# Optimization experiments

Measured on AMD Instinct MI355X. Metric: run time of the kernel, lower is better.

## Reference

```python
import jax, jax.numpy as jnp
import numpy as np

LN_EPS = 1e-5

def layer_norm(x, g, b):
    mu = jnp.mean(x, axis=-1, keepdims=True)
    var = jnp.var(x, axis=-1, keepdims=True)
    return (x - mu) * jax.lax.rsqrt(var + LN_EPS) * g + b

def setup_inputs() -> dict:
    key = jax.random.key(0)
    ks = jax.random.split(key, 4)
    d = 2048
    bs, win_len, obj_num = 8, 64, 36
    return {
        "visual_feats": jax.random.normal(ks[0], (bs, win_len, d), dtype=jnp.float32),
        "obj_feats": jax.random.normal(ks[1], (bs, win_len, obj_num, d), dtype=jnp.float32),
        "W_v": jax.random.normal(ks[2], (d, d), dtype=jnp.float32) * (1.0 / np.sqrt(d)),
        "b_v": jnp.zeros((d,), dtype=jnp.float32),
        "W_o": jax.random.normal(ks[3], (d, d), dtype=jnp.float32) * (1.0 / np.sqrt(d)),
        "b_o": jnp.zeros((d,), dtype=jnp.float32),
        "ln_v_g": jnp.ones((d,), dtype=jnp.float32),
        "ln_v_b": jnp.zeros((d,), dtype=jnp.float32),
        "ln_o_g": jnp.ones((d,), dtype=jnp.float32),
        "ln_o_b": jnp.zeros((d,), dtype=jnp.float32),
        "ln_ov_g": jnp.ones((d,), dtype=jnp.float32),
        "ln_ov_b": jnp.zeros((d,), dtype=jnp.float32),
    }

def reference(visual_feats, obj_feats, W_v, b_v, W_o, b_o,
              ln_v_g, ln_v_b, ln_o_g, ln_o_b, ln_ov_g, ln_ov_b):
    bs, win_len, obj_num, obj_size = obj_feats.shape
    # visual branch: linear -> tanh -> LN   [bs, F, d]
    ve = layer_norm(jnp.tanh(visual_feats @ W_v + b_v), ln_v_g, ln_v_b)
    # object branch: linear -> flatten frames*objects -> tanh -> LN  [bs, N, d]
    oe = (obj_feats @ W_o + b_o).reshape(bs, win_len * obj_num, obj_size)
    oe = layer_norm(jnp.tanh(oe), ln_o_g, ln_o_b)
    # adjacency: [bs, N, F], softmax over N (object axis, dim=1)
    adj = jnp.einsum('bnd,bfd->bnf', oe, ve) / jnp.sqrt(jnp.asarray(obj_size, dtype=oe.dtype))
    adj = jax.nn.softmax(adj, axis=1)
    # aggregate objects per frame: (oe^T @ adj)^T -> [bs, F, d]
    obj_agg = jnp.einsum('bnd,bnf->bfd', oe, adj)
    return layer_norm(jnp.tanh(obj_agg + ve), ln_ov_g, ln_ov_b)
```

## Files before the change

### kernel.cpp

```cpp
#include <hip/hip_runtime.h>
#include <cstdint>
#include <cstddef>


typedef __attribute__((ext_vector_type(4))) float f32x4;
typedef __attribute__((ext_vector_type(4))) unsigned int u32x4;
typedef __attribute__((ext_vector_type(8))) short bf16x8;

#define DD 2048
#define BS 8
#define FF 64
#define NOBJ 2304
#define MO 18432
#define MV 512

__device__ __forceinline__ unsigned short f2bf(float f) {
  unsigned int u = __float_as_uint(f);
  u += 0x7fffu + ((u >> 16) & 1u);
  return (unsigned short)(u >> 16);
}
__device__ __forceinline__ unsigned int pk2(float a, float b) {
  return (unsigned int)f2bf(a) | ((unsigned int)f2bf(b) << 16);
}
__device__ __forceinline__ float bf2f(unsigned short u) {
  return __uint_as_float((unsigned int)u << 16);
}

typedef __attribute__((address_space(1))) const unsigned int gas_u32;
typedef __attribute__((address_space(3))) unsigned int las_u32;
__device__ __forceinline__ void gl_lds16(const void* g, void* l) {
  __builtin_amdgcn_global_load_lds((gas_u32*)g, (las_u32*)l, 16, 0, 0);
}

__global__ __launch_bounds__(256) void k_cvt_bf16(const float* __restrict__ X,
                                                  unsigned short* __restrict__ O,
                                                  int n16) {
  int idx = blockIdx.x * 256 + threadIdx.x;
  const int stride = gridDim.x * 256;
  for (int i = idx; i < n16; i += stride) {
    const f32x4* src = (const f32x4*)(X + (size_t)i * 16);
    f32x4 a = src[0], b = src[1], c = src[2], d = src[3];
    u32x4 p = {pk2(a.x, a.y), pk2(a.z, a.w), pk2(b.x, b.y), pk2(b.z, b.w)};
    u32x4 q = {pk2(c.x, c.y), pk2(c.z, c.w), pk2(d.x, d.y), pk2(d.z, d.w)};
    u32x4* dst = (u32x4*)(O + (size_t)i * 16);
    dst[0] = p;
    dst[1] = q;
  }
}

__global__ __launch_bounds__(256) void k_wprep(const float* __restrict__ W,
                                               unsigned short* __restrict__ Wt) {
  __shared__ unsigned short sh[64][65];
  const int t = threadIdx.x;
  const int kb = blockIdx.x * 64, nb = blockIdx.y * 64;
  {
    const int rk = t >> 2, seg = t & 3;
    const float* src = W + (size_t)(kb + rk) * DD + nb + seg * 16;
#pragma unroll
    for (int q = 0; q < 4; ++q) {
      f32x4 x = *(const f32x4*)(src + q * 4);
      sh[rk][seg * 16 + q * 4 + 0] = f2bf(x.x);
      sh[rk][seg * 16 + q * 4 + 1] = f2bf(x.y);
      sh[rk][seg * 16 + q * 4 + 2] = f2bf(x.z);
      sh[rk][seg * 16 + q * 4 + 3] = f2bf(x.w);
    }
  }
  __syncthreads();
  {
    const int nn = t >> 2, ks = t & 3;
    unsigned int o[8];
#pragma unroll
    for (int j = 0; j < 8; ++j)
      o[j] = (unsigned int)sh[ks * 16 + 2 * j][nn] |
             ((unsigned int)sh[ks * 16 + 2 * j + 1][nn] << 16);
    u32x4 p0 = {o[0], o[1], o[2], o[3]};
    u32x4 p1 = {o[4], o[5], o[6], o[7]};
    unsigned short* dst = Wt + (size_t)(nb + nn) * DD + kb + ks * 16;
    ((u32x4*)dst)[0] = p0;
    ((u32x4*)dst)[1] = p1;
  }
}

__global__ __launch_bounds__(512, 1) void k_gemm_bbf(const unsigned short* __restrict__ A,
                                                     const unsigned short* __restrict__ Bt,
                                                     const float* __restrict__ bias,
                                                     unsigned short* __restrict__ T,
                                                     float* __restrict__ part) {
  __shared__ __align__(16) unsigned short lds[2 * 32768];
  const int tid = threadIdx.x;
  const int lane = tid & 63, wave = tid >> 6;
  const int r = lane & 15, g = lane >> 4;
  const int wm = wave >> 2, wn = wave & 3;

  const int orig = blockIdx.y * 8 + blockIdx.x;
  const int lin = (orig & 7) * 72 + (orig >> 3);
  const int bm = (lin >> 3) * 256;
  const int bn = (lin & 7) * 256;

  const int srow = tid >> 3;
  const int k16s = (tid & 7) ^ (srow & 7);
  const unsigned short* aS = A + (size_t)(bm + srow) * DD + k16s * 8;
  const unsigned short* bS = Bt + (size_t)(bn + srow) * DD + k16s * 8;

  auto stage = [&](int buf, int kt) {
    unsigned short* ab = lds + buf * 32768;
    unsigned short* bb = ab + 16384;
    const size_t ko = (size_t)kt * 64;
#pragma unroll
    for (int i = 0; i < 4; ++i)
      gl_lds16(aS + ko + (size_t)(i * 64) * DD, ab + ((i * 512 + tid) << 3));
#pragma unroll
    for (int i = 0; i < 4; ++i)
      gl_lds16(bS + ko + (size_t)(i * 64) * DD, bb + ((i * 512 + tid) << 3));
  };

  const int rs = r & 7;
  const int s0 = ((0 + g) ^ rs) * 8;
  const int s1 = ((4 + g) ^ rs) * 8;
  const int abase = (wm * 128 + r) * 64;
  const int bbase = 16384 + (wn * 64 + r) * 64;

  f32x4 acc[8][4] = {};

  stage(0, 0);
  asm volatile("s_waitcnt vmcnt(0)" ::: "memory");
  __builtin_amdgcn_s_barrier();

  for (int kt = 0; kt < DD / 64; ++kt) {
    const unsigned short* bufp = lds + (kt & 1) * 32768;
    const bool st = (kt + 1 < DD / 64);

#define PHASE(QA, QB, DOSTAGE, DOWAIT)                                         \
    {                                                                          \
      bf16x8 af[4][2], bfv[2][2];                                              \
      _Pragma("unroll")                                                        \
      for (int mi = 0; mi < 4; ++mi) {                                         \
        const int ro = abase + ((QA) * 64 + mi * 16) * 64;                     \
        af[mi][0] = *(const bf16x8*)(bufp + ro + s0);                          \
        af[mi][1] = *(const bf16x8*)(bufp + ro + s1);                          \
      }                                                                        \
      _Pragma("unroll")                                                        \
      for (int ni = 0; ni < 2; ++ni) {                                         \
        const int ro = bbase + ((QB) * 32 + ni * 16) * 64;                     \
        bfv[ni][0] = *(const bf16x8*)(bufp + ro + s0);                         \
        bfv[ni][1] = *(const bf16x8*)(bufp + ro + s1);                         \
      }                                                                        \
      if (DOSTAGE) stage((kt + 1) & 1, kt + 1);                                \
      __builtin_amdgcn_s_barrier();                                            \
      __builtin_amdgcn_s_setprio(1);                                           \
      _Pragma("unroll")                                                        \
      for (int mi = 0; mi < 4; ++mi)                                           \
        _Pragma("unroll")                                                      \
        for (int ni = 0; ni < 2; ++ni) {                                       \
          acc[(QA) * 4 + mi][(QB) * 2 + ni] = __builtin_amdgcn_mfma_f32_16x16x32_bf16( \
              af[mi][0], bfv[ni][0], acc[(QA) * 4 + mi][(QB) * 2 + ni], 0, 0, 0);      \
          acc[(QA) * 4 + mi][(QB) * 2 + ni] = __builtin_amdgcn_mfma_f32_16x16x32_bf16( \
              af[mi][1], bfv[ni][1], acc[(QA) * 4 + mi][(QB) * 2 + ni], 0, 0, 0);      \
        }                                                                      \
      __builtin_amdgcn_s_setprio(0);                                           \
      if (DOWAIT) asm volatile("s_waitcnt vmcnt(0)" ::: "memory");             \
      __builtin_amdgcn_s_barrier();                                            \
    }

    PHASE(0, 0, st, false)
    PHASE(0, 1, false, false)
    PHASE(1, 0, false, false)
    PHASE(1, 1, false, st)
#undef PHASE
  }

  float bv[4];
#pragma unroll
  for (int ni = 0; ni < 4; ++ni) bv[ni] = bias[bn + wn * 64 + ni * 16 + r];
  const int slot = ((lin & 7) << 2) + wn;
#pragma unroll
  for (int mi = 0; mi < 8; ++mi) {
#pragma unroll
    for (int i2 = 0; i2 < 4; ++i2) {
      const int row = bm + wm * 128 + mi * 16 + g * 4 + i2;
      unsigned short* trow = T + (size_t)row * DD + bn + wn * 64 + r;
      float s1 = 0.f, s2 = 0.f;
#pragma unroll
      for (int ni = 0; ni < 4; ++ni) {
        const float tv = tanhf(acc[mi][ni][i2] + bv[ni]);
        trow[ni * 16] = f2bf(tv);
        s1 += tv;
        s2 += tv * tv;
      }
#pragma unroll
      for (int m = 1; m < 16; m <<= 1) {
        s1 += __shfl_xor(s1, m, 64);
        s2 += __shfl_xor(s2, m, 64);
      }
      if (r == 0) {
        float2 p2 = make_float2(s1, s2);
        *(float2*)(part + (size_t)row * 64 + slot * 2) = p2;
      }
    }
  }
}

__global__ __launch_bounds__(256) void k_ep_ln2(const unsigned short* __restrict__ T,
                                                const float* __restrict__ part,
                                                const float* __restrict__ gw,
                                                const float* __restrict__ bw,
                                                unsigned short* __restrict__ obf) {
  const int row = blockIdx.x, t = threadIdx.x;
  float s1 = 0.f, s2 = 0.f;
  if (t < 32) {
    float2 p = ((const float2*)(part + (size_t)row * 64))[t];
    s1 = p.x;
    s2 = p.y;
  }
#pragma unroll
  for (int m = 1; m < 64; m <<= 1) {
    s1 += __shfl_xor(s1, m, 64);
    s2 += __shfl_xor(s2, m, 64);
  }
  __shared__ float sh[2];
  if (t == 0) {
    sh[0] = s1;
    sh[1] = s2;
  }
  __syncthreads();
  const float mean = sh[0] * (1.0f / DD);
  const float var = sh[1] * (1.0f / DD) - mean * mean;
  const float rstd = rsqrtf(var + 1e-5f);
  const size_t base = (size_t)row * DD + t * 8;
  u32x4 tin = *(const u32x4*)(T + base);
  f32x4 g0 = ((const f32x4*)(gw + t * 8))[0], g1 = ((const f32x4*)(gw + t * 8))[1];
  f32x4 bb0 = ((const f32x4*)(bw + t * 8))[0], bb1 = ((const f32x4*)(bw + t * 8))[1];
  float gv[8], bvv[8];
  gv[0] = g0.x; gv[1] = g0.y; gv[2] = g0.z; gv[3] = g0.w;
  gv[4] = g1.x; gv[5] = g1.y; gv[6] = g1.z; gv[7] = g1.w;
  bvv[0] = bb0.x; bvv[1] = bb0.y; bvv[2] = bb0.z; bvv[3] = bb0.w;
  bvv[4] = bb1.x; bvv[5] = bb1.y; bvv[6] = bb1.z; bvv[7] = bb1.w;
  float o[8];
#pragma unroll
  for (int j = 0; j < 4; ++j) {
    const float tl = bf2f((unsigned short)(tin[j] & 0xffffu));
    const float th = bf2f((unsigned short)(tin[j] >> 16));
    o[2 * j] = (tl - mean) * rstd * gv[2 * j] + bvv[2 * j];
    o[2 * j + 1] = (th - mean) * rstd * gv[2 * j + 1] + bvv[2 * j + 1];
  }
  u32x4 p = {pk2(o[0], o[1]), pk2(o[2], o[3]), pk2(o[4], o[5]), pk2(o[6], o[7])};
  *((u32x4*)(obf + base)) = p;
}

__global__ __launch_bounds__(256) void k_gemm_xw(const float* __restrict__ X,
                                                 const unsigned short* __restrict__ Wt,
                                                 const float* __restrict__ bias,
                                                 float* __restrict__ Y) {
  __shared__ __align__(16) unsigned short As[128 * 32];
  __shared__ __align__(16) unsigned short Bs[128 * 32];
  const int t = threadIdx.x;
  const int lane = t & 63, wave = t >> 6;
  const int r = lane & 15, g = lane >> 4;
  const int wm = wave >> 1, wn = wave & 1;
  const int bm = blockIdx.y * 128, bn = blockIdx.x * 128;
  const int arow = t >> 1, ah = t & 1;
  f32x4 acc[4][4] = {};
  const float* aptr = X + (size_t)(bm + arow) * DD + ah * 16;
  const unsigned short* bptr = Wt + (size_t)(bn + arow) * DD + ah * 16;
  for (int kt = 0; kt < DD / 32; ++kt) {
    const int kb = kt * 32;
    f32x4 a0 = *(const f32x4*)(aptr + kb);
    f32x4 a1 = *(const f32x4*)(aptr + kb + 4);
    f32x4 a2 = *(const f32x4*)(aptr + kb + 8);
    f32x4 a3 = *(const f32x4*)(aptr + kb + 12);
    u32x4 b0 = *(const u32x4*)(bptr + kb);
    u32x4 b1 = *(const u32x4*)(bptr + kb + 8);
    __syncthreads();
    u32x4 p0 = {pk2(a0.x, a0.y), pk2(a0.z, a0.w), pk2(a1.x, a1.y), pk2(a1.z, a1.w)};
    u32x4 p1 = {pk2(a2.x, a2.y), pk2(a2.z, a2.w), pk2(a3.x, a3.y), pk2(a3.z, a3.w)};
    ((u32x4*)As)[arow * 4 + ah * 2 + 0] = p0;
    ((u32x4*)As)[arow * 4 + ah * 2 + 1] = p1;
    ((u32x4*)Bs)[arow * 4 + ah * 2 + 0] = b0;
    ((u32x4*)Bs)[arow * 4 + ah * 2 + 1] = b1;
    __syncthreads();
    bf16x8 af[4], bfr[4];
#pragma unroll
    for (int m = 0; m < 4; ++m) af[m] = ((const bf16x8*)As)[(wm * 64 + m * 16 + r) * 4 + g];
#pragma unroll
    for (int n = 0; n < 4; ++n) bfr[n] = ((const bf16x8*)Bs)[(wn * 64 + n * 16 + r) * 4 + g];
#pragma unroll
    for (int m = 0; m < 4; ++m)
#pragma unroll
      for (int n = 0; n < 4; ++n)
        acc[m][n] = __builtin_amdgcn_mfma_f32_16x16x32_bf16(af[m], bfr[n], acc[m][n], 0, 0, 0);
  }
#pragma unroll
  for (int m = 0; m < 4; ++m) {
    const int row0 = bm + wm * 64 + m * 16 + g * 4;
#pragma unroll
    for (int n = 0; n < 4; ++n) {
      const int col = bn + wn * 64 + n * 16 + r;
      const float bvx = bias[col];
#pragma unroll
      for (int i = 0; i < 4; ++i)
        Y[(size_t)(row0 + i) * DD + col] = acc[m][n][i] + bvx;
    }
  }
}

__global__ __launch_bounds__(256) void k_ep_ln(const float* __restrict__ Y,
                                               const float* __restrict__ Y2,
                                               const float* __restrict__ gw,
                                               const float* __restrict__ bw,
                                               unsigned short* __restrict__ obf,
                                               float* __restrict__ of32) {
  const int row = blockIdx.x, t = threadIdx.x;
  const size_t base = (size_t)row * DD + t * 8;
  f32x4 v0 = ((const f32x4*)(Y + base))[0];
  f32x4 v1 = ((const f32x4*)(Y + base))[1];
  if (Y2 != nullptr) {
    v0 += ((const f32x4*)(Y2 + base))[0];
    v1 += ((const f32x4*)(Y2 + base))[1];
  }
  float tv[8];
#pragma unroll
  for (int j = 0; j < 4; ++j) {
    tv[j] = tanhf(v0[j]);
    tv[4 + j] = tanhf(v1[j]);
  }
  float s1 = 0.f, s2 = 0.f;
#pragma unroll
  for (int j = 0; j < 8; ++j) {
    s1 += tv[j];
    s2 += tv[j] * tv[j];
  }
#pragma unroll
  for (int m = 1; m < 64; m <<= 1) {
    s1 += __shfl_xor(s1, m, 64);
    s2 += __shfl_xor(s2, m, 64);
  }
  __shared__ float r1[4], r2[4];
  const int wave = t >> 6;
  if ((t & 63) == 0) {
    r1[wave] = s1;
    r2[wave] = s2;
  }
  __syncthreads();
  const float S1 = r1[0] + r1[1] + r1[2] + r1[3];
  const float S2 = r2[0] + r2[1] + r2[2] + r2[3];
  const float mean = S1 * (1.0f / DD);
  const float var = S2 * (1.0f / DD) - mean * mean;
  const float rstd = rsqrtf(var + 1e-5f);
  f32x4 g0 = ((const f32x4*)(gw + t * 8))[0], g1 = ((const f32x4*)(gw + t * 8))[1];
  f32x4 bb0 = ((const f32x4*)(bw + t * 8))[0], bb1 = ((const f32x4*)(bw + t * 8))[1];
  float o[8];
#pragma unroll
  for (int j = 0; j < 4; ++j) {
    o[j] = (tv[j] - mean) * rstd * g0[j] + bb0[j];
    o[4 + j] = (tv[4 + j] - mean) * rstd * g1[j] + bb1[j];
  }
  if (obf != nullptr) {
    u32x4 p = {pk2(o[0], o[1]), pk2(o[2], o[3]), pk2(o[4], o[5]), pk2(o[6], o[7])};
    *((u32x4*)(obf + base)) = p;
  }
  if (of32 != nullptr) {
    f32x4 w0 = {o[0], o[1], o[2], o[3]}, w1 = {o[4], o[5], o[6], o[7]};
    ((f32x4*)(of32 + base))[0] = w0;
    ((f32x4*)(of32 + base))[1] = w1;
  }
}

__global__ __launch_bounds__(256) void k_troe(const unsigned short* __restrict__ oe,
                                              unsigned short* __restrict__ oeT) {
  __shared__ unsigned short sh[64][65];
  const int t = threadIdx.x;
  const int b = blockIdx.z, nt = blockIdx.x, dt = blockIdx.y;
  {
    const int nn = t >> 2, seg = t & 3;
    const unsigned short* src = oe + ((size_t)b * NOBJ + nt * 64 + nn) * DD + dt * 64 + seg * 16;
    u32x4 x0 = ((const u32x4*)src)[0];
    u32x4 x1 = ((const u32x4*)src)[1];
    const unsigned short* px0 = (const unsigned short*)&x0;
    const unsigned short* px1 = (const unsigned short*)&x1;
#pragma unroll
    for (int j = 0; j < 8; ++j) {
      sh[nn][seg * 16 + j] = px0[j];
      sh[nn][seg * 16 + 8 + j] = px1[j];
    }
  }
  __syncthreads();
  {
    const int dd = t >> 2, ns = t & 3;
    unsigned int o[8];
#pragma unroll
    for (int j = 0; j < 8; ++j)
      o[j] = (unsigned int)sh[ns * 16 + 2 * j][dd] |
             ((unsigned int)sh[ns * 16 + 2 * j + 1][dd] << 16);
    u32x4 p0 = {o[0], o[1], o[2], o[3]};
    u32x4 p1 = {o[4], o[5], o[6], o[7]};
    unsigned short* dst = oeT + ((size_t)b * DD + dt * 64 + dd) * NOBJ + nt * 64 + ns * 16;
    ((u32x4*)dst)[0] = p0;
    ((u32x4*)dst)[1] = p1;
  }
}

__global__ __launch_bounds__(256) void k_gemm_adj(const unsigned short* __restrict__ oe,
                                                  const unsigned short* __restrict__ veb,
                                                  float* __restrict__ adjT) {
  __shared__ __align__(16) unsigned short As[128 * 32];
  __shared__ __align__(16) unsigned short Bs[64 * 32];
  const int t = threadIdx.x;
  const int lane = t & 63, wave = t >> 6;
  const int r = lane & 15, g = lane >> 4;
  const int wm = wave >> 1, wn = wave & 1;
  const int b = blockIdx.y, bm = blockIdx.x * 128;
  const int arow = t >> 1, ah = t & 1;
  const int br_ = t >> 2, bseg = t & 3;
  f32x4 acc[4][2] = {};
  const unsigned short* aptr = oe + ((size_t)b * NOBJ + bm + arow) * DD + ah * 16;
  const unsigned short* bptr = veb + ((size_t)b * FF + br_) * DD + bseg * 8;
  for (int kt = 0; kt < DD / 32; ++kt) {
    const int kb = kt * 32;
    u32x4 a0 = ((const u32x4*)(aptr + kb))[0];
    u32x4 a1 = ((const u32x4*)(aptr + kb))[1];
    u32x4 bvx = *(const u32x4*)(bptr + kb);
    __syncthreads();
    ((u32x4*)As)[arow * 4 + ah * 2 + 0] = a0;
    ((u32x4*)As)[arow * 4 + ah * 2 + 1] = a1;
    ((u32x4*)Bs)[br_ * 4 + bseg] = bvx;
    __syncthreads();
    bf16x8 af[4], bfr[2];
#pragma unroll
    for (int m = 0; m < 4; ++m) af[m] = ((const bf16x8*)As)[(wm * 64 + m * 16 + r) * 4 + g];
#pragma unroll
    for (int n = 0; n < 2; ++n) bfr[n] = ((const bf16x8*)Bs)[(wn * 32 + n * 16 + r) * 4 + g];
#pragma unroll
    for (int m = 0; m < 4; ++m)
#pragma unroll
      for (int n = 0; n < 2; ++n)
        acc[m][n] = __builtin_amdgcn_mfma_f32_16x16x32_bf16(af[m], bfr[n], acc[m][n], 0, 0, 0);
  }
  const float scale = 0.02209708691207961f;
#pragma unroll
  for (int m = 0; m < 4; ++m)
#pragma unroll
    for (int n = 0; n < 2; ++n) {
      const int f = wn * 32 + n * 16 + r;
      const int n0 = bm + wm * 64 + m * 16 + g * 4;
      f32x4 v = acc[m][n];
      v *= scale;
      *(f32x4*)(adjT + ((size_t)b * FF + f) * NOBJ + n0) = v;
    }
}

__global__ __launch_bounds__(256) void k_smax(const float* __restrict__ adjT,
                                              unsigned short* __restrict__ out) {
  const int t = threadIdx.x;
  const size_t base = (size_t)blockIdx.x * NOBJ;
  float v[9];
#pragma unroll
  for (int j = 0; j < 9; ++j) v[j] = adjT[base + t + j * 256];
  float m = v[0];
#pragma unroll
  for (int j = 1; j < 9; ++j) m = fmaxf(m, v[j]);
#pragma unroll
  for (int s = 1; s < 64; s <<= 1) m = fmaxf(m, __shfl_xor(m, s, 64));
  __shared__ float rm[4], rs[4];
  const int wave = t >> 6;
  if ((t & 63) == 0) rm[wave] = m;
  __syncthreads();
  m = fmaxf(fmaxf(rm[0], rm[1]), fmaxf(rm[2], rm[3]));
  float e[9];
  float s = 0.f;
#pragma unroll
  for (int j = 0; j < 9; ++j) {
    e[j] = __expf(v[j] - m);
    s += e[j];
  }
#pragma unroll
  for (int q = 1; q < 64; q <<= 1) s += __shfl_xor(s, q, 64);
  if ((t & 63) == 0) rs[wave] = s;
  __syncthreads();
  const float S = rs[0] + rs[1] + rs[2] + rs[3];
  const float inv = 1.0f / S;
#pragma unroll
  for (int j = 0; j < 9; ++j) out[base + t + j * 256] = f2bf(e[j] * inv);
}

__global__ __launch_bounds__(256) void k_gemm_agg(const unsigned short* __restrict__ adjsm,
                                                  const unsigned short* __restrict__ oeT,
                                                  float* __restrict__ agg) {
  __shared__ __align__(16) unsigned short As[64 * 32];
  __shared__ __align__(16) unsigned short Bs[128 * 32];
  const int t = threadIdx.x;
  const int lane = t & 63, wave = t >> 6;
  const int r = lane & 15, g = lane >> 4;
  const int wm = wave >> 1, wn = wave & 1;
  const int b = blockIdx.y, bn = blockIdx.x * 128;
  const int ar = t >> 2, aseg = t & 3;
  const int brow = t >> 1, bh = t & 1;
  f32x4 acc[2][4] = {};
  const unsigned short* aptr = adjsm + ((size_t)b * FF + ar) * NOBJ + aseg * 8;
  const unsigned short* bptr = oeT + ((size_t)b * DD + bn + brow) * NOBJ + bh * 16;
  for (int kt = 0; kt < NOBJ / 32; ++kt) {
    const int kb = kt * 32;
    u32x4 av = *(const u32x4*)(aptr + kb);
    u32x4 b0 = ((const u32x4*)(bptr + kb))[0];
    u32x4 b1 = ((const u32x4*)(bptr + kb))[1];
    __syncthreads();
    ((u32x4*)As)[ar * 4 + aseg] = av;
    ((u32x4*)Bs)[brow * 4 + bh * 2 + 0] = b0;
    ((u32x4*)Bs)[brow * 4 + bh * 2 + 1] = b1;
    __syncthreads();
    bf16x8 af[2], bfr[4];
#pragma unroll
    for (int m = 0; m < 2; ++m) af[m] = ((const bf16x8*)As)[(wm * 32 + m * 16 + r) * 4 + g];
#pragma unroll
    for (int n = 0; n < 4; ++n) bfr[n] = ((const bf16x8*)Bs)[(wn * 64 + n * 16 + r) * 4 + g];
#pragma unroll
    for (int m = 0; m < 2; ++m)
#pragma unroll
      for (int n = 0; n < 4; ++n)
        acc[m][n] = __builtin_amdgcn_mfma_f32_16x16x32_bf16(af[m], bfr[n], acc[m][n], 0, 0, 0);
  }
#pragma unroll
  for (int m = 0; m < 2; ++m)
#pragma unroll
    for (int n = 0; n < 4; ++n) {
      const int d = bn + wn * 64 + n * 16 + r;
#pragma unroll
      for (int i = 0; i < 4; ++i) {
        const int f = wm * 32 + m * 16 + g * 4 + i;
        agg[((size_t)b * FF + f) * DD + d] = acc[m][n][i];
      }
    }
}


extern "C" void kernel_launch(void* const* d_in, const int* in_sizes, int n_in,
                              void* d_out, int out_size, void* d_ws, size_t ws_size,
                              hipStream_t stream) {
  (void)in_sizes; (void)n_in; (void)out_size;
  const float* visual = (const float*)d_in[0];
  const float* obj    = (const float*)d_in[1];
  const float* W_v    = (const float*)d_in[2];
  const float* b_v    = (const float*)d_in[3];
  const float* W_o    = (const float*)d_in[4];
  const float* b_o    = (const float*)d_in[5];
  const float* ln_v_g = (const float*)d_in[6];
  const float* ln_v_b = (const float*)d_in[7];
  const float* ln_o_g = (const float*)d_in[8];
  const float* ln_o_b = (const float*)d_in[9];
  const float* ln_ov_g = (const float*)d_in[10];
  const float* ln_ov_b = (const float*)d_in[11];

  char* ws = (char*)d_ws;
  constexpr size_t OFF_WVT = 0;
  constexpr size_t OFF_WOT = 8ull << 20;
  constexpr size_t OFF_OBJB = 16ull << 20;
  constexpr size_t OFF_T   = 88ull << 20;
  constexpr size_t OFF_PART = 160ull << 20;
  constexpr size_t OFF_YV  = 232ull << 20;
  constexpr size_t OFF_VEF = 236ull << 20;
  constexpr size_t OFF_VEB = 240ull << 20;
  constexpr size_t OFF_ADJ = 242ull << 20;
  constexpr size_t OFF_ADJS = OFF_ADJ + 4718592ull;
  constexpr size_t OFF_AGG = OFF_ADJS + 2359296ull;
  constexpr size_t WS_NEED = OFF_AGG + 4194304ull;
  if (ws_size < WS_NEED) return;

  unsigned short* WvT  = (unsigned short*)(ws + OFF_WVT);
  unsigned short* WoT  = (unsigned short*)(ws + OFF_WOT);
  unsigned short* objb = (unsigned short*)(ws + OFF_OBJB);
  unsigned short* oe_b = (unsigned short*)(ws + OFF_OBJB);
  unsigned short* T    = (unsigned short*)(ws + OFF_T);
  unsigned short* oeT  = (unsigned short*)(ws + OFF_T);
  float* part          = (float*)(ws + OFF_PART);
  float* Yv            = (float*)(ws + OFF_YV);
  float* ve_f          = (float*)(ws + OFF_VEF);
  unsigned short* ve_b = (unsigned short*)(ws + OFF_VEB);
  float* adjT          = (float*)(ws + OFF_ADJ);
  unsigned short* adjs = (unsigned short*)(ws + OFF_ADJS);
  float* agg           = (float*)(ws + OFF_AGG);

  dim3 b256(256);
  k_wprep<<<dim3(32, 32), b256, 0, stream>>>(W_v, WvT);
  k_wprep<<<dim3(32, 32), b256, 0, stream>>>(W_o, WoT);
  k_cvt_bf16<<<dim3(2048), b256, 0, stream>>>(obj, objb, MO * DD / 16);
  k_gemm_xw<<<dim3(16, MV / 128), b256, 0, stream>>>(visual, WvT, b_v, Yv);
  k_gemm_bbf<<<dim3(8, MO / 256), dim3(512), 0, stream>>>(objb, WoT, b_o, T, part);
  k_ep_ln<<<dim3(MV), b256, 0, stream>>>(Yv, nullptr, ln_v_g, ln_v_b, ve_b, ve_f);
  k_ep_ln2<<<dim3(MO), b256, 0, stream>>>(T, part, ln_o_g, ln_o_b, oe_b);
  k_troe<<<dim3(36, 32, 8), b256, 0, stream>>>(oe_b, oeT);
  k_gemm_adj<<<dim3(NOBJ / 128, BS), b256, 0, stream>>>(oe_b, ve_b, adjT);
  k_smax<<<dim3(MV), b256, 0, stream>>>(adjT, adjs);
  k_gemm_agg<<<dim3(DD / 128, BS), b256, 0, stream>>>(adjs, oeT, agg);
  k_ep_ln<<<dim3(MV), b256, 0, stream>>>(agg, ve_f, ln_ov_g, ln_ov_b, nullptr, (float*)d_out);
}
```

Measured before the change: 538.2 us.

## Restructure big GEMM k-loop to one barrier per tile and merge weight-prep launches

The main object GEMM k-loop drops its four-phase pattern, which placed two barriers around each quarter. It now issues the next-tile prefetch up front, loads all B fragments once, and sweeps the A quarters with a single barrier per k-tile. This cuts synchronisation overhead and reloads of B fragments, at the cost of more live registers and less fine-grained interleaving of LDS reads with MFMA work. The two weight-conversion kernels are also merged into one launch using a z grid dimension.

```diff
diff --git a/kernel.cpp b/kernel.cpp
--- a/kernel.cpp
+++ b/kernel.cpp
@@ -48,9 +48,13 @@
   }
 }
 
-__global__ __launch_bounds__(256) void k_wprep(const float* __restrict__ W,
-                                               unsigned short* __restrict__ Wt) {
+__global__ __launch_bounds__(256) void k_wprep2(const float* __restrict__ Wv,
+                                                const float* __restrict__ Wo,
+                                                unsigned short* __restrict__ WvT,
+                                                unsigned short* __restrict__ WoT) {
   __shared__ unsigned short sh[64][65];
+  const float* W = blockIdx.z ? Wo : Wv;
+  unsigned short* Wt = blockIdx.z ? WoT : WvT;
   const int t = threadIdx.x;
   const int kb = blockIdx.x * 64, nb = blockIdx.y * 64;
   {
@@ -129,44 +133,38 @@
   for (int kt = 0; kt < DD / 64; ++kt) {
     const unsigned short* bufp = lds + (kt & 1) * 32768;
     const bool st = (kt + 1 < DD / 64);
-
-#define PHASE(QA, QB, DOSTAGE, DOWAIT)                                         \
-    {                                                                          \
-      bf16x8 af[4][2], bfv[2][2];                                              \
-      _Pragma("unroll")                                                        \
-      for (int mi = 0; mi < 4; ++mi) {                                         \
-        const int ro = abase + ((QA) * 64 + mi * 16) * 64;                     \
-        af[mi][0] = *(const bf16x8*)(bufp + ro + s0);                          \
-        af[mi][1] = *(const bf16x8*)(bufp + ro + s1);                          \
-      }                                                                        \
-      _Pragma("unroll")                                                        \
-      for (int ni = 0; ni < 2; ++ni) {                                         \
-        const int ro = bbase + ((QB) * 32 + ni * 16) * 64;                     \
-        bfv[ni][0] = *(const bf16x8*)(bufp + ro + s0);                         \
-        bfv[ni][1] = *(const bf16x8*)(bufp + ro + s1);                         \
-      }                                                                        \
-      if (DOSTAGE) stage((kt + 1) & 1, kt + 1);                                \
-      __builtin_amdgcn_s_barrier();                                            \
-      __builtin_amdgcn_s_setprio(1);                                           \
-      _Pragma("unroll")                                                        \
-      for (int mi = 0; mi < 4; ++mi)                                           \
-        _Pragma("unroll")                                                      \
-        for (int ni = 0; ni < 2; ++ni) {                                       \
-          acc[(QA) * 4 + mi][(QB) * 2 + ni] = __builtin_amdgcn_mfma_f32_16x16x32_bf16( \
-              af[mi][0], bfv[ni][0], acc[(QA) * 4 + mi][(QB) * 2 + ni], 0, 0, 0);      \
-          acc[(QA) * 4 + mi][(QB) * 2 + ni] = __builtin_amdgcn_mfma_f32_16x16x32_bf16( \
-              af[mi][1], bfv[ni][1], acc[(QA) * 4 + mi][(QB) * 2 + ni], 0, 0, 0);      \
-        }                                                                      \
-      __builtin_amdgcn_s_setprio(0);                                           \
-      if (DOWAIT) asm volatile("s_waitcnt vmcnt(0)" ::: "memory");             \
-      __builtin_amdgcn_s_barrier();                                            \
-    }
-
-    PHASE(0, 0, st, false)
-    PHASE(0, 1, false, false)
-    PHASE(1, 0, false, false)
-    PHASE(1, 1, false, st)
-#undef PHASE
+    if (st) stage((kt + 1) & 1, kt + 1);
+
+    bf16x8 bAll[4][2];
+#pragma unroll
+    for (int ni = 0; ni < 4; ++ni) {
+      const int ro = bbase + ni * 1024;
+      bAll[ni][0] = *(const bf16x8*)(bufp + ro + s0);
+      bAll[ni][1] = *(const bf16x8*)(bufp + ro + s1);
+    }
+#pragma unroll
+    for (int q = 0; q < 4; ++q) {
+      bf16x8 af[2][2];
+#pragma unroll
+      for (int mi = 0; mi < 2; ++mi) {
+        const int ro = abase + (q * 32 + mi * 16) * 64;
+        af[mi][0] = *(const bf16x8*)(bufp + ro + s0);
+        af[mi][1] = *(const bf16x8*)(bufp + ro + s1);
+      }
+      __builtin_amdgcn_s_setprio(1);
+#pragma unroll
+      for (int mi = 0; mi < 2; ++mi)
+#pragma unroll
+        for (int ni = 0; ni < 4; ++ni) {
+          acc[q * 2 + mi][ni] = __builtin_amdgcn_mfma_f32_16x16x32_bf16(
+              af[mi][0], bAll[ni][0], acc[q * 2 + mi][ni], 0, 0, 0);
+          acc[q * 2 + mi][ni] = __builtin_amdgcn_mfma_f32_16x16x32_bf16(
+              af[mi][1], bAll[ni][1], acc[q * 2 + mi][ni], 0, 0, 0);
+        }
+      __builtin_amdgcn_s_setprio(0);
+    }
+    if (st) asm volatile("s_waitcnt vmcnt(0)" ::: "memory");
+    __builtin_amdgcn_s_barrier();
   }
 
   float bv[4];
@@ -579,8 +577,7 @@
   float* agg           = (float*)(ws + OFF_AGG);
 
   dim3 b256(256);
-  k_wprep<<<dim3(32, 32), b256, 0, stream>>>(W_v, WvT);
-  k_wprep<<<dim3(32, 32), b256, 0, stream>>>(W_o, WoT);
+  k_wprep2<<<dim3(32, 32, 2), b256, 0, stream>>>(W_v, W_o, WvT, WoT);
   k_cvt_bf16<<<dim3(2048), b256, 0, stream>>>(obj, objb, MO * DD / 16);
   k_gemm_xw<<<dim3(16, MV / 128), b256, 0, stream>>>(visual, WvT, b_v, Yv);
   k_gemm_bbf<<<dim3(8, MO / 256), dim3(512), 0, stream>>>(objb, WoT, b_o, T, part);
```

Measured after the change: 487.3 us. 9.5% less time.
